# Performance work log

Measured on AMD Instinct MI355X. Metric: run time of the kernel, lower is better.

Reference implementation:

```python
import jax, jax.numpy as jnp
import numpy as np

B, J, HID, INTER, NL = 4096, 16, 128, 64, 4
NEG = -9.0e15
EDGES = [(0,1),(1,2),(2,3),(0,4),(4,5),(5,6),(0,7),(7,8),(8,9),(8,10),(10,11),(11,12),(8,13),(13,14),(14,15)]
GROUPED = [0,7,1,4,2,5,3,6,8,10,9,13,11,14,12,15]  # flattened nodes_group


def _adjacency_nonzeros():
    A = np.zeros((J, J), np.float32)
    for i, j in EDGES:
        A[i, j] = 1.0
        A[j, i] = 1.0
    A += np.eye(J, dtype=np.float32)
    rows, cols = np.nonzero(A)  # row-major, matches torch adj[mask] = e fill order
    return rows.astype(np.int32), cols.astype(np.int32)


def setup_inputs() -> dict:
    key = jax.random.key(0)
    ks = iter(jax.random.split(key, 64))
    rn = lambda shape, s: jax.random.normal(next(ks), shape, jnp.float32) * s
    rows, cols = _adjacency_nonzeros()
    nnz = rows.shape[0]  # 46
    inp = dict(
        x=jax.random.normal(next(ks), (B, J, 2), jnp.float32),
        # input SemGraphConv (2 -> HID) + its BatchNorm
        gc_in_W=rn((2, 2, HID), 0.7), gc_in_e=1.0 + rn((nnz,), 0.3), gc_in_b=rn((HID,), 0.05),
        bn_in_g=1.0 + rn((HID,), 0.05), bn_in_b=rn((HID,), 0.05),
        # 4 residual blocks x 2 graph convs (HID -> HID)
        W_res=rn((2 * NL, 2, HID, HID), 0.08), e_res=1.0 + rn((2 * NL, nnz), 0.3),
        b_res=rn((2 * NL, HID), 0.05),
        bng_res=1.0 + rn((2 * NL, HID), 0.05), bnb_res=rn((2 * NL, HID), 0.05),
        # 5 GraphNonLocal blocks (1 after input + 1 per residual block)
        nl_g_w=rn((NL + 1, INTER, HID), 0.08), nl_g_b=rn((NL + 1, INTER), 0.05),
        nl_t_w=rn((NL + 1, INTER, HID), 0.08), nl_t_b=rn((NL + 1, INTER), 0.05),
        nl_p_w=rn((NL + 1, INTER, HID), 0.08), nl_p_b=rn((NL + 1, INTER), 0.05),
        nl_cp_w=rn((NL + 1, 2 * INTER), 0.08),  # concat_project 1x1 conv, no bias
        nl_W_w=rn((NL + 1, HID, INTER), 0.08), nl_W_b=rn((NL + 1, HID), 0.05),
        nl_bn_g=1.0 + rn((NL + 1, HID), 0.05), nl_bn_b=rn((NL + 1, HID), 0.05),
        # output SemGraphConv (HID -> 3)
        gc_out_W=rn((2, HID, 3), 0.08), gc_out_e=1.0 + rn((nnz,), 0.3), gc_out_b=rn((3,), 0.05),
        # integer constants
        mask_rows=jnp.asarray(rows), mask_cols=jnp.asarray(cols),
        grouped_order=jnp.asarray(GROUPED, jnp.int32),
        restored_order=jnp.asarray(np.argsort(GROUPED), jnp.int32),
    )
    return inp


def reference(x, gc_in_W, gc_in_e, gc_in_b, bn_in_g, bn_in_b,
              W_res, e_res, b_res, bng_res, bnb_res,
              nl_g_w, nl_g_b, nl_t_w, nl_t_b, nl_p_w, nl_p_b,
              nl_cp_w, nl_W_w, nl_W_b, nl_bn_g, nl_bn_b,
              gc_out_W, gc_out_e, gc_out_b,
              mask_rows, mask_cols, grouped_order, restored_order):
    eye = jnp.eye(J, dtype=x.dtype)

    def gconv(h, W, e, b):
        # h: [B, J, F]
        h0 = jnp.einsum('bjf,fo->bjo', h, W[0])
        h1 = jnp.einsum('bjf,fo->bjo', h, W[1])
        logits = jnp.full((J, J), NEG, h.dtype).at[mask_rows, mask_cols].set(e)
        adj = jax.nn.softmax(logits, axis=1)
        diag = jnp.diagonal(adj)                     # adj*I picks diagonal scaling
        off = adj * (1.0 - eye)
        return diag[None, :, None] * h0 + jnp.einsum('ij,bjo->bio', off, h1) + b

    def bn(h, g, bta, axes):
        # training-mode BatchNorm (biased variance), per-channel
        m = h.mean(axes, keepdims=True)
        v = h.var(axes, keepdims=True)
        return (h - m) * jax.lax.rsqrt(v + 1e-5) * g + bta

    def graph_conv(h, W, e, b, gm, gb):
        h = gconv(h, W, e, b)
        h = bn(h, gm[None, None, :], gb[None, None, :], (0, 1))
        return jax.nn.relu(h)

    def nonlocal_block(h, i):
        xo = h[:, grouped_order]          # [B, J, C] regroup joints
        xc = xo.transpose(0, 2, 1)        # [B, C, J]
        conv = lambda w, bb: jnp.einsum('oc,bcj->boj', w, xc) + bb[None, :, None]
        pool = lambda t: t.reshape(B, INTER, J // 2, 2).max(-1)   # MaxPool1d(k=2)
        gx = pool(conv(nl_g_w[i], nl_g_b[i]))                     # [B, I, J/2]
        th = conv(nl_t_w[i], nl_t_b[i])                           # [B, I, J]
        ph = pool(conv(nl_p_w[i], nl_p_b[i]))                     # [B, I, J/2]
        wt, wp = nl_cp_w[i][:INTER], nl_cp_w[i][INTER:]
        # concat_project 1x1 conv over concat(theta,phi) decomposes into a sum
        f = jax.nn.relu(jnp.einsum('bch,c->bh', th, wt)[:, :, None]
                        + jnp.einsum('bcw,c->bw', ph, wp)[:, None, :])  # [B, J, J/2]
        f = f / (J // 2)
        y = jnp.einsum('bhw,bcw->bch', f, gx)                     # [B, I, J]
        Wy = jnp.einsum('oc,bch->boh', nl_W_w[i], y) + nl_W_b[i][None, :, None]
        Wy = bn(Wy, nl_bn_g[i][None, :, None], nl_bn_b[i][None, :, None], (0, 2))
        z = Wy + xc
        return z.transpose(0, 2, 1)[:, restored_order]

    out = graph_conv(x, gc_in_W, gc_in_e, gc_in_b, bn_in_g, bn_in_b)
    out = nonlocal_block(out, 0)
    for i in range(NL):
        res = out
        out = graph_conv(out, W_res[2 * i], e_res[2 * i], b_res[2 * i], bng_res[2 * i], bnb_res[2 * i])
        out = graph_conv(out, W_res[2 * i + 1], e_res[2 * i + 1], b_res[2 * i + 1], bng_res[2 * i + 1], bnb_res[2 * i + 1])
        out = res + out
        out = nonlocal_block(out, i + 1)
    return gconv(out, gc_out_W, gc_out_e, gc_out_b)  # [B, J, 3]
```

## Files before the change

kernel.cpp:

```cpp
#include <hip/hip_runtime.h>

#define B 4096
#define J 16
#define HID 128
#define INTER 64
#define NLAYERS 4
#define NEGV -9000000000000000.0f
#define ELEMS ((size_t)B*16*128)
#define NREP 16
#define SLOT 4096

typedef __attribute__((ext_vector_type(8))) short short8;
typedef __attribute__((ext_vector_type(4))) float f32x4;

static __device__ __forceinline__ unsigned short f2bf(float x) {
    unsigned u = __float_as_uint(x);
    unsigned r = u + 0x7fffu + ((u >> 16) & 1u);
    return (unsigned short)(r >> 16);
}
static __device__ __forceinline__ void splitbf(float x, unsigned short& h, unsigned short& l) {
    h = f2bf(x);
    float hf = __uint_as_float((unsigned)h << 16);
    l = f2bf(x - hf);
}
static __device__ __forceinline__ void splitbf4(float4 v, uint2& hh, uint2& ll) {
    unsigned short h0,l0,h1,l1,h2,l2,h3,l3;
    splitbf(v.x,h0,l0); splitbf(v.y,h1,l1); splitbf(v.z,h2,l2); splitbf(v.w,h3,l3);
    hh = make_uint2((unsigned)h0 | ((unsigned)h1<<16), (unsigned)h2 | ((unsigned)h3<<16));
    ll = make_uint2((unsigned)l0 | ((unsigned)l1<<16), (unsigned)l2 | ((unsigned)l3<<16));
}
static __device__ __forceinline__ f32x4 mfma16(short8 a, short8 b, f32x4 c) {
    return __builtin_amdgcn_mfma_f32_16x16x32_bf16(a, b, c, 0, 0, 0);
}
static __device__ __forceinline__ f32x4 mfma_split(short8 ah, short8 al,
                                                   short8 bh, short8 bl, f32x4 acc) {
    acc = mfma16(ah, bh, acc);
    acc = mfma16(ah, bl, acc);
    acc = mfma16(al, bh, acc);
    return acc;
}
static __device__ __forceinline__ float bfpair(unsigned short h, unsigned short l) {
    return __uint_as_float((unsigned)h << 16) + __uint_as_float((unsigned)l << 16);
}

__global__ void adj_kernel(const float* __restrict__ e_in,
                           const float* __restrict__ e_res,
                           const float* __restrict__ e_out,
                           const int* __restrict__ rows,
                           const int* __restrict__ cols, int nnz,
                           float* __restrict__ off_all,
                           float* __restrict__ diag_all) {
    int m = blockIdx.x;
    int i = threadIdx.x;
    const float* e = (m == 0) ? e_in : (m <= 8) ? e_res + (size_t)(m - 1) * nnz : e_out;
    float l[16];
    for (int j = 0; j < 16; j++) l[j] = NEGV;
    for (int k = 0; k < nnz; k++)
        if (rows[k] == i) l[cols[k]] = e[k];
    float mx = l[0];
    for (int j = 1; j < 16; j++) mx = fmaxf(mx, l[j]);
    float ex[16], s = 0.f;
    for (int j = 0; j < 16; j++) { ex[j] = expf(l[j] - mx); s += ex[j]; }
    float inv = 1.f / s;
    for (int j = 0; j < 16; j++) {
        float a = ex[j] * inv;
        if (j == i) { diag_all[m * 16 + i] = a; a = 0.f; }
        off_all[m * 256 + i * 16 + j] = a;
    }
}

#define WB_N   262144
#define NLW_N  122880
#define NLWW_N 40960
__global__ void prep_w_kernel(const float* __restrict__ W_res,
                              const float* __restrict__ g_w, const float* __restrict__ t_w,
                              const float* __restrict__ p_w, const float* __restrict__ W_w,
                              unsigned short* __restrict__ Wbh, unsigned short* __restrict__ Wbl,
                              unsigned short* __restrict__ nlwh, unsigned short* __restrict__ nlwl,
                              unsigned short* __restrict__ nlWh, unsigned short* __restrict__ nlWl) {
    int i = blockIdx.x * 256 + threadIdx.x;
    unsigned short h, l;
    if (i < WB_N) {
        int lay = i >> 15, rem = i & 32767, n = rem >> 8, k = rem & 255;
        int d = k >> 7, f = k & 127;
        splitbf(W_res[(((lay << 1) | d) * 128 + f) * 128 + n], h, l);
        Wbh[i] = h; Wbl[i] = l;
    } else if (i < WB_N + NLW_N) {
        int j = i - WB_N;
        int lay = j / 24576, r2 = j % 24576;
        int conv = r2 >> 13, oc = r2 & 8191;
        const float* src = conv == 0 ? g_w : conv == 1 ? t_w : p_w;
        splitbf(src[lay * 8192 + oc], h, l);
        nlwh[j] = h; nlwl[j] = l;
    } else if (i < WB_N + NLW_N + NLWW_N) {
        int j = i - WB_N - NLW_N;
        splitbf(W_w[j], h, l);
        nlWh[j] = h; nlWl[j] = l;
    }
}

__global__ void prep_vt_kernel(const float* __restrict__ t_w, const float* __restrict__ t_b,
                               const float* __restrict__ cp_w,
                               float* __restrict__ vt, float* __restrict__ ct) {
    int l = blockIdx.x, c = threadIdx.x;
    float s = 0.f;
    for (int c2 = 0; c2 < 64; c2++)
        s += cp_w[l * 128 + c2] * t_w[(l * 64 + c2) * 128 + c];
    vt[l * 128 + c] = s;
    if (c == 0) {
        float s2 = 0.f;
        for (int c2 = 0; c2 < 64; c2++) s2 += cp_w[l * 128 + c2] * t_b[l * 64 + c2];
        ct[l] = s2;
    }
}

__global__ void finalize_kernel(const float* __restrict__ slot, float* __restrict__ fin) {
    __shared__ float sh[256];
    int t = threadIdx.x;
    float s = 0.f;
    #pragma unroll
    for (int r = 0; r < NREP; r++) s += slot[r * 256 + t];
    sh[t] = s;
    __syncthreads();
    if (t < 128) {
        float m = sh[t] * (1.f / 65536.f);
        float v = sh[128 + t] * (1.f / 65536.f) - m * m;
        fin[t] = m;
        fin[128 + t] = rsqrtf(v + 1e-5f);
    }
}

__global__ __launch_bounds__(256) void gconv_in_kernel(
        const float* __restrict__ x, const float* __restrict__ W,
        const float* __restrict__ bias, const float* __restrict__ off,
        const float* __restrict__ diag, float* __restrict__ out,
        float* __restrict__ stats_out) {
    __shared__ float xs[16][2];
    __shared__ float gs[16][2];
    __shared__ float red[512];
    int b = blockIdx.x, t = threadIdx.x;
    if (t < 32) xs[t >> 1][t & 1] = x[b * 32 + t];
    __syncthreads();
    if (t < 32) {
        int i = t >> 1, f = t & 1;
        float g = 0.f;
        #pragma unroll
        for (int j = 0; j < 16; j++) g += off[i * 16 + j] * xs[j][f];
        gs[i][f] = g;
    }
    __syncthreads();
    int o = t & 127;
    float w00 = W[o], w01 = W[128 + o], w10 = W[256 + o], w11 = W[384 + o], bo = bias[o];
    float s = 0.f, q = 0.f;
    for (int idx = t; idx < 2048; idx += 256) {
        int i = idx >> 7;
        float v = diag[i] * (xs[i][0] * w00 + xs[i][1] * w01)
                + gs[i][0] * w10 + gs[i][1] * w11 + bo;
        out[(size_t)b * 2048 + idx] = v;
        s += v; q += v * v;
    }
    red[t] = s; red[256 + t] = q;
    __syncthreads();
    float* so = stats_out + (b & (NREP - 1)) * 256;
    if (t < 128) {
        atomicAdd(&so[t], red[t] + red[t + 128]);
        atomicAdd(&so[128 + t], red[256 + t] + red[256 + t + 128]);
    }
}

__global__ __launch_bounds__(256) void gconv_mfma_kernel(
        const float* src, const float* wy,
        const float* __restrict__ fin,
        const float* __restrict__ bn_g, const float* __restrict__ bn_b,
        const int* __restrict__ restored, float* zdst,
        const unsigned short* __restrict__ Wbh,
        const unsigned short* __restrict__ Wbl,
        const float* __restrict__ bias,
        const float* __restrict__ off, const float* __restrict__ diag,
        float* dst, float* __restrict__ stats_out) {
    __shared__ float hraw[16][132];
    __shared__ __align__(16) unsigned short ksh[16][264];
    __shared__ __align__(16) unsigned short ksl[16][264];
    __shared__ float offs[256];
    __shared__ float diags[16];
    int t = threadIdx.x;
    offs[t] = off[t];
    if (t < 16) diags[t] = diag[t];
    int c4 = (4 * t) & 127;
    int r0 = t >> 5;
    float4 m4 = make_float4(0,0,0,0), sc4 = make_float4(0,0,0,0), bb4 = make_float4(0,0,0,0);
    if (fin) {
        m4 = *(const float4*)&fin[c4];
        float4 iv = *(const float4*)&fin[128 + c4];
        float4 g4 = *(const float4*)&bn_g[c4];
        bb4 = *(const float4*)&bn_b[c4];
        sc4 = make_float4(iv.x * g4.x, iv.y * g4.y, iv.z * g4.z, iv.w * g4.w);
    }
    int ro0 = 0, ro1 = 0;
    if (wy) { ro0 = restored[r0]; ro1 = restored[r0 + 8]; }
    int b0 = blockIdx.x;
    const float4* src4 = (const float4*)src;
    const float4* wy4  = (const float4*)wy;
    float4 sv0 = src4[(size_t)b0 * 512 + t];
    float4 sv1 = src4[(size_t)b0 * 512 + 256 + t];
    float4 wv0 = make_float4(0,0,0,0), wv1 = make_float4(0,0,0,0);
    if (wy) {
        wv0 = wy4[(size_t)b0 * 512 + ro0 * 32 + (c4 >> 2)];
        wv1 = wy4[(size_t)b0 * 512 + ro1 * 32 + (c4 >> 2)];
    }
    int wv_ = t >> 6, lane = t & 63;
    int mn = lane & 15, kq = (lane >> 4) << 3, qr = (lane >> 4) << 2;

    for (int s = 0; s < 2; s++) {
        int bb_ = blockIdx.x + s * 2048;
        {
            float4 v = sv0;
            if (wy) {
                v.x += (wv0.x - m4.x) * sc4.x + bb4.x;
                v.y += (wv0.y - m4.y) * sc4.y + bb4.y;
                v.z += (wv0.z - m4.z) * sc4.z + bb4.z;
                v.w += (wv0.w - m4.w) * sc4.w + bb4.w;
                ((float4*)zdst)[(size_t)bb_ * 512 + t] = v;
            } else if (fin) {
                v.x = fmaxf((v.x - m4.x) * sc4.x + bb4.x, 0.f);
                v.y = fmaxf((v.y - m4.y) * sc4.y + bb4.y, 0.f);
                v.z = fmaxf((v.z - m4.z) * sc4.z + bb4.z, 0.f);
                v.w = fmaxf((v.w - m4.w) * sc4.w + bb4.w, 0.f);
            }
            *(float4*)&hraw[r0][c4] = v;
            v = sv1;
            if (wy) {
                v.x += (wv1.x - m4.x) * sc4.x + bb4.x;
                v.y += (wv1.y - m4.y) * sc4.y + bb4.y;
                v.z += (wv1.z - m4.z) * sc4.z + bb4.z;
                v.w += (wv1.w - m4.w) * sc4.w + bb4.w;
                ((float4*)zdst)[(size_t)bb_ * 512 + 256 + t] = v;
            } else if (fin) {
                v.x = fmaxf((v.x - m4.x) * sc4.x + bb4.x, 0.f);
                v.y = fmaxf((v.y - m4.y) * sc4.y + bb4.y, 0.f);
                v.z = fmaxf((v.z - m4.z) * sc4.z + bb4.z, 0.f);
                v.w = fmaxf((v.w - m4.w) * sc4.w + bb4.w, 0.f);
            }
            *(float4*)&hraw[r0 + 8][c4] = v;
        }
        if (s == 0) {
            int b1 = blockIdx.x + 2048;
            sv0 = src4[(size_t)b1 * 512 + t];
            sv1 = src4[(size_t)b1 * 512 + 256 + t];
            if (wy) {
                wv0 = wy4[(size_t)b1 * 512 + ro0 * 32 + (c4 >> 2)];
                wv1 = wy4[(size_t)b1 * 512 + ro1 * 32 + (c4 >> 2)];
            }
        }
        __syncthreads();
        for (int u = t; u < 512; u += 256) {
            int i = u >> 5, f4 = (u & 31) << 2;
            float4 hv = *(const float4*)&hraw[i][f4];
            float4 g = make_float4(0.f, 0.f, 0.f, 0.f);
            #pragma unroll
            for (int j = 0; j < 16; j++) {
                float w = offs[i * 16 + j];
                float4 hj = *(const float4*)&hraw[j][f4];
                g.x += w * hj.x; g.y += w * hj.y; g.z += w * hj.z; g.w += w * hj.w;
            }
            float d = diags[i];
            uint2 hh, ll;
            splitbf4(make_float4(d * hv.x, d * hv.y, d * hv.z, d * hv.w), hh, ll);
            *(uint2*)&ksh[i][f4] = hh;
            *(uint2*)&ksl[i][f4] = ll;
            splitbf4(g, hh, ll);
            *(uint2*)&ksh[i][128 + f4] = hh;
            *(uint2*)&ksl[i][128 + f4] = ll;
        }
        __syncthreads();
        int n0 = wv_ << 5;
        f32x4 acc0 = {0.f, 0.f, 0.f, 0.f}, acc1 = {0.f, 0.f, 0.f, 0.f};
        const unsigned short* wh0 = Wbh + (size_t)(n0 + mn) * 256 + kq;
        const unsigned short* wl0 = Wbl + (size_t)(n0 + mn) * 256 + kq;
        #pragma unroll
        for (int k = 0; k < 8; k++) {
            int k0 = k << 5;
            short8 ah = *(const short8*)&ksh[mn][k0 + kq];
            short8 al = *(const short8*)&ksl[mn][k0 + kq];
            acc0 = mfma_split(ah, al, *(const short8*)(wh0 + k0), *(const short8*)(wl0 + k0), acc0);
            acc1 = mfma_split(ah, al, *(const short8*)(wh0 + 4096 + k0), *(const short8*)(wl0 + 4096 + k0), acc1);
        }
        float bias0 = bias[n0 + mn], bias1 = bias[n0 + 16 + mn];
        float s0 = 0.f, q0 = 0.f, s1 = 0.f, q1 = 0.f;
        #pragma unroll
        for (int r = 0; r < 4; r++) {
            int row = qr + r;
            float v0 = acc0[r] + bias0;
            float v1 = acc1[r] + bias1;
            dst[(size_t)bb_ * 2048 + row * 128 + n0 + mn] = v0;
            dst[(size_t)bb_ * 2048 + row * 128 + n0 + 16 + mn] = v1;
            s0 += v0; q0 += v0 * v0; s1 += v1; q1 += v1 * v1;
        }
        s0 += __shfl_xor(s0, 16); s0 += __shfl_xor(s0, 32);
        q0 += __shfl_xor(q0, 16); q0 += __shfl_xor(q0, 32);
        s1 += __shfl_xor(s1, 16); s1 += __shfl_xor(s1, 32);
        q1 += __shfl_xor(q1, 16); q1 += __shfl_xor(q1, 32);
        float* so = stats_out + (bb_ & (NREP - 1)) * 256;
        if (lane < 16) {
            atomicAdd(&so[n0 + mn], s0);
            atomicAdd(&so[128 + n0 + mn], q0);
            atomicAdd(&so[n0 + 16 + mn], s1);
            atomicAdd(&so[128 + n0 + 16 + mn], q1);
        }
        if (s == 0) __syncthreads();
    }
}

#define CG(conv, o, j) cgbuf[((conv) * 64 + (o)) * 17 + (j)]
#define WYL(o, j)      cgbuf[(o) * 17 + (j)]
__global__ __launch_bounds__(256) void nl_a_kernel(
        const float* tsrc, const float* __restrict__ fin,
        const float* __restrict__ bn_g, const float* __restrict__ bn_b,
        const float* res,
        const unsigned short* __restrict__ nlwh,
        const unsigned short* __restrict__ nlwl,
        const float* __restrict__ g_b, const float* __restrict__ p_b,
        const float* __restrict__ cpw,
        const float* __restrict__ vt, const float* __restrict__ ctp,
        const unsigned short* __restrict__ nlWh,
        const unsigned short* __restrict__ nlWl,
        const float* __restrict__ W_b,
        const int* __restrict__ restored,
        float* hdst, float* wydst, float* __restrict__ wst) {
    __shared__ __align__(16) unsigned short xch[16][136];
    __shared__ __align__(16) unsigned short xcl[16][136];
    __shared__ float cgbuf[2176];
    __shared__ float gx[64][9];
    __shared__ float tvp[16][4], pvp[8][8];
    __shared__ float tv[16], pv[8];
    __shared__ float vtl[128];
    __shared__ __align__(16) unsigned short ybh[16][72];
    __shared__ __align__(16) unsigned short ybl[16][72];
    int b = blockIdx.x, t = threadIdx.x;
    {
        if (t < 128) vtl[t] = vt[t];
        int c4 = (4 * t) & 127;
        float4 m4 = *(const float4*)&fin[c4];
        float4 iv = *(const float4*)&fin[128 + c4];
        float4 g4 = *(const float4*)&bn_g[c4];
        float4 bb4 = *(const float4*)&bn_b[c4];
        float4 sc4 = make_float4(iv.x * g4.x, iv.y * g4.y, iv.z * g4.z, iv.w * g4.w);
        int r0 = t >> 5;
        #pragma unroll
        for (int u = 0; u < 2; u++) {
            int fi = t + 256 * u;
            int r = r0 + 8 * u;
            float4 v = ((const float4*)tsrc)[(size_t)b * 512 + fi];
            v.x = fmaxf((v.x - m4.x) * sc4.x + bb4.x, 0.f);
            v.y = fmaxf((v.y - m4.y) * sc4.y + bb4.y, 0.f);
            v.z = fmaxf((v.z - m4.z) * sc4.z + bb4.z, 0.f);
            v.w = fmaxf((v.w - m4.w) * sc4.w + bb4.w, 0.f);
            if (res) {
                float4 rv = ((const float4*)res)[(size_t)b * 512 + fi];
                v.x += rv.x; v.y += rv.y; v.z += rv.z; v.w += rv.w;
            }
            ((float4*)hdst)[(size_t)b * 512 + fi] = v;
            int rg = restored[r];
            uint2 hh, ll;
            splitbf4(v, hh, ll);
            *(uint2*)&xch[rg][c4] = hh;
            *(uint2*)&xcl[rg][c4] = ll;
        }
    }
    __syncthreads();
    int wv = t >> 6, lane = t & 63;
    int mn = lane & 15, kq = (lane >> 4) << 3, qr = (lane >> 4) << 2;
    {
        short8 bh[4], bl[4];
        #pragma unroll
        for (int s = 0; s < 4; s++) {
            bh[s] = *(const short8*)&xch[mn][s * 32 + kq];
            bl[s] = *(const short8*)&xcl[mn][s * 32 + kq];
        }
        #pragma unroll
        for (int jj = 0; jj < 2; jj++) {
            int jb = wv + jj * 4;
            int conv = jb >> 2;
            int mt = jb & 3;
            int wbase = (conv == 0) ? 0 : 128;
            const unsigned short* aph = nlwh + (size_t)(wbase + mt * 16 + mn) * 128 + kq;
            const unsigned short* apl = nlwl + (size_t)(wbase + mt * 16 + mn) * 128 + kq;
            f32x4 acc = {0.f, 0.f, 0.f, 0.f};
            #pragma unroll
            for (int s = 0; s < 4; s++)
                acc = mfma_split(*(const short8*)(aph + s * 32), *(const short8*)(apl + s * 32),
                                 bh[s], bl[s], acc);
            const float* bias = (conv == 0) ? g_b : p_b;
            #pragma unroll
            for (int r = 0; r < 4; r++) {
                int o = mt * 16 + qr + r;
                CG(conv, o, mn) = acc[r] + bias[o];
            }
        }
    }
    __syncthreads();
    if (t < 128) {
        for (int u = t; u < 512; u += 128) {
            int c = u >> 3, w2 = u & 7;
            gx[c][w2] = fmaxf(CG(0, c, 2 * w2), CG(0, c, 2 * w2 + 1));
        }
    } else if (t < 192) {
        int u = t - 128, w2 = u & 7, ch = u >> 3;
        float s = 0.f;
        for (int c = ch * 8; c < ch * 8 + 8; c++)
            s += fmaxf(CG(1, c, 2 * w2), CG(1, c, 2 * w2 + 1)) * cpw[64 + c];
        pvp[w2][ch] = s;
    } else {
        int u = t - 192, j = u & 15, ch = u >> 4;
        float s = 0.f;
        int c0 = ch * 32;
        for (int c = c0; c < c0 + 32; c += 2) {
            unsigned hh = *(const unsigned*)&xch[j][c];
            unsigned ll = *(const unsigned*)&xcl[j][c];
            float v0 = bfpair((unsigned short)hh, (unsigned short)ll);
            float v1 = bfpair((unsigned short)(hh >> 16), (unsigned short)(ll >> 16));
            s += vtl[c] * v0 + vtl[c + 1] * v1;
        }
        tvp[j][ch] = s;
    }
    __syncthreads();
    if (t < 16) {
        tv[t] = tvp[t][0] + tvp[t][1] + tvp[t][2] + tvp[t][3] + ctp[0];
    } else if (t < 24) {
        int w2 = t - 16;
        float s = 0.f;
        #pragma unroll
        for (int ch = 0; ch < 8; ch++) s += pvp[w2][ch];
        pv[w2] = s;
    }
    __syncthreads();
    for (int u = t; u < 1024; u += 256) {
        int j = u >> 6, c = u & 63;
        float s = 0.f;
        #pragma unroll
        for (int w2 = 0; w2 < 8; w2++)
            s += fmaxf(tv[j] + pv[w2], 0.f) * gx[c][w2];
        unsigned short h, l;
        splitbf(s * 0.125f, h, l);
        ybh[j][c] = h; ybl[j][c] = l;
    }
    __syncthreads();
    {
        short8 byh0 = *(const short8*)&ybh[mn][kq];
        short8 byh1 = *(const short8*)&ybh[mn][32 + kq];
        short8 byl0 = *(const short8*)&ybl[mn][kq];
        short8 byl1 = *(const short8*)&ybl[mn][32 + kq];
        #pragma unroll
        for (int mm = 0; mm < 2; mm++) {
            int mt = wv * 2 + mm;
            const unsigned short* aph = nlWh + (size_t)(mt * 16 + mn) * 64 + kq;
            const unsigned short* apl = nlWl + (size_t)(mt * 16 + mn) * 64 + kq;
            f32x4 acc = {0.f, 0.f, 0.f, 0.f};
            acc = mfma_split(*(const short8*)aph, *(const short8*)apl, byh0, byl0, acc);
            acc = mfma_split(*(const short8*)(aph + 32), *(const short8*)(apl + 32), byh1, byl1, acc);
            #pragma unroll
            for (int r = 0; r < 4; r++) {
                int o = mt * 16 + qr + r;
                WYL(o, mn) = acc[r] + W_b[o];
            }
        }
    }
    __syncthreads();
    {
        int c = t & 127;
        float s = 0.f, q = 0.f;
        for (int idx = t; idx < 2048; idx += 256) {
            int j = idx >> 7;
            float v = WYL(c, j);
            wydst[(size_t)b * 2048 + idx] = v;
            s += v; q += v * v;
        }
        float* red = &gx[0][0];
        red[t] = s; red[256 + t] = q;
        __syncthreads();
        float* so = wst + (b & (NREP - 1)) * 256;
        if (t < 128) {
            atomicAdd(&so[t], red[t] + red[t + 128]);
            atomicAdd(&so[128 + t], red[256 + t] + red[256 + t + 128]);
        }
    }
}

__global__ __launch_bounds__(256) void gconv_out_kernel(
        const float* __restrict__ h, const float* __restrict__ wy,
        const float* __restrict__ fin,
        const float* __restrict__ nlg, const float* __restrict__ nlb,
        const int* __restrict__ restored,
        const float* __restrict__ W,
        const float* __restrict__ bias, const float* __restrict__ off,
        const float* __restrict__ diag, float* __restrict__ out) {
    __shared__ float hs[16][132];
    __shared__ float gsv[16][132];
    __shared__ float offs[256];
    __shared__ float p0[48][4], p1[48][4];
    int b = blockIdx.x, t = threadIdx.x;
    offs[t] = off[t];
    {
        int c = t & 127;
        float mean = fin[c];
        float inv = fin[128 + c] * nlg[c];
        float bb = nlb[c];
        for (int idx = t; idx < 2048; idx += 256) {
            int r = idx >> 7;
            float wval = wy[(size_t)b * 2048 + restored[r] * 128 + c];
            hs[r][c] = (wval - mean) * inv + bb + h[(size_t)b * 2048 + idx];
        }
    }
    __syncthreads();
    for (int idx = t; idx < 2048; idx += 256) {
        int i = idx >> 7, f = idx & 127;
        float g = 0.f;
        #pragma unroll
        for (int j = 0; j < 16; j++) g += offs[i * 16 + j] * hs[j][f];
        gsv[i][f] = g;
    }
    __syncthreads();
    if (t < 192) {
        int oid = t >> 2, chunk = t & 3;
        int i = oid / 3, o = oid % 3;
        float a0 = 0.f, a1 = 0.f;
        int f0 = chunk * 32;
        for (int f = f0; f < f0 + 32; f++) {
            a0 += hs[i][f] * W[f * 3 + o];
            a1 += gsv[i][f] * W[384 + f * 3 + o];
        }
        p0[oid][chunk] = a0; p1[oid][chunk] = a1;
    }
    __syncthreads();
    if (t < 48) {
        int i = t / 3, o = t % 3;
        float a0 = p0[t][0] + p0[t][1] + p0[t][2] + p0[t][3];
        float a1 = p1[t][0] + p1[t][1] + p1[t][2] + p1[t][3];
        out[(size_t)b * 48 + t] = diag[i] * a0 + a1 + bias[o];
    }
}

extern "C" void kernel_launch(void* const* d_in, const int* in_sizes, int n_in,
                              void* d_out, int out_size, void* d_ws, size_t ws_size,
                              hipStream_t stream) {
    (void)n_in; (void)out_size; (void)ws_size;
    const float* x        = (const float*)d_in[0];
    const float* gc_in_W  = (const float*)d_in[1];
    const float* gc_in_e  = (const float*)d_in[2];
    const float* gc_in_b  = (const float*)d_in[3];
    const float* bn_in_g  = (const float*)d_in[4];
    const float* bn_in_b  = (const float*)d_in[5];
    const float* W_res    = (const float*)d_in[6];
    const float* e_res    = (const float*)d_in[7];
    const float* b_res    = (const float*)d_in[8];
    const float* bng_res  = (const float*)d_in[9];
    const float* bnb_res  = (const float*)d_in[10];
    const float* nl_g_w   = (const float*)d_in[11];
    const float* nl_g_b   = (const float*)d_in[12];
    const float* nl_t_w   = (const float*)d_in[13];
    const float* nl_t_b   = (const float*)d_in[14];
    const float* nl_p_w   = (const float*)d_in[15];
    const float* nl_p_b   = (const float*)d_in[16];
    const float* nl_cp_w  = (const float*)d_in[17];
    const float* nl_W_w   = (const float*)d_in[18];
    const float* nl_W_b   = (const float*)d_in[19];
    const float* nl_bn_g  = (const float*)d_in[20];
    const float* nl_bn_b  = (const float*)d_in[21];
    const float* gc_out_W = (const float*)d_in[22];
    const float* gc_out_e = (const float*)d_in[23];
    const float* gc_out_b = (const float*)d_in[24];
    const int*   mask_rows = (const int*)d_in[25];
    const int*   mask_cols = (const int*)d_in[26];
    const int*   restored  = (const int*)d_in[28];
    int nnz = in_sizes[2];

    float* ws       = (float*)d_ws;
    float* off_all  = ws;
    float* diag_all = ws + 2560;
    float* stats    = ws + 2720;
    float* fin      = ws + 60064;
    float* vt       = ws + 63664;
    float* ct       = ws + 64304;
    unsigned short* Wbh  = (unsigned short*)(ws + 65536);
    unsigned short* Wbl  = Wbh + WB_N;
    unsigned short* nlwh = Wbl + WB_N;
    unsigned short* nlwl = nlwh + NLW_N;
    unsigned short* nlWh = nlwl + NLW_N;
    unsigned short* nlWl = nlWh + NLWW_N;
    float* Z = ws + 491520;
    float* T = Z + ELEMS;

    hipMemsetAsync(stats, 0, 14 * SLOT * sizeof(float), stream);
    adj_kernel<<<10, 16, 0, stream>>>(gc_in_e, e_res, gc_out_e, mask_rows, mask_cols,
                                      nnz, off_all, diag_all);
    prep_w_kernel<<<(WB_N + NLW_N + NLWW_N + 255) / 256, 256, 0, stream>>>(
        W_res, nl_g_w, nl_t_w, nl_p_w, nl_W_w, Wbh, Wbl, nlwh, nlwl, nlWh, nlWl);
    prep_vt_kernel<<<5, 128, 0, stream>>>(nl_t_w, nl_t_b, nl_cp_w, vt, ct);

    gconv_in_kernel<<<B, 256, 0, stream>>>(x, gc_in_W, gc_in_b, off_all, diag_all,
                                           T, stats);
    finalize_kernel<<<1, 256, 0, stream>>>(stats, fin);
    nl_a_kernel<<<B, 256, 0, stream>>>(T, fin, bn_in_g, bn_in_b, nullptr,
                                       nlwh, nlwl, nl_g_b, nl_p_b, nl_cp_w,
                                       vt, ct, nlWh, nlWl, nl_W_b, restored,
                                       Z, T, stats + SLOT);
    finalize_kernel<<<1, 256, 0, stream>>>(stats + SLOT, fin + 256);

    int sl = 1;
    for (int i = 0; i < NLAYERS; i++) {
        int l0 = 2 * i, l1 = 2 * i + 1, li = i + 1;
        gconv_mfma_kernel<<<2048, 256, 0, stream>>>(
            Z, T, fin + (size_t)sl * 256,
            nl_bn_g + i * 128, nl_bn_b + i * 128, restored, Z,
            Wbh + (size_t)l0 * 32768, Wbl + (size_t)l0 * 32768, b_res + l0 * 128,
            off_all + (1 + l0) * 256, diag_all + (1 + l0) * 16, T,
            stats + (size_t)(sl + 1) * SLOT);
        finalize_kernel<<<1, 256, 0, stream>>>(stats + (size_t)(sl + 1) * SLOT,
                                               fin + (size_t)(sl + 1) * 256);
        gconv_mfma_kernel<<<2048, 256, 0, stream>>>(
            T, nullptr, fin + (size_t)(sl + 1) * 256,
            bng_res + l0 * 128, bnb_res + l0 * 128, nullptr, nullptr,
            Wbh + (size_t)l1 * 32768, Wbl + (size_t)l1 * 32768, b_res + l1 * 128,
            off_all + (1 + l1) * 256, diag_all + (1 + l1) * 16, T,
            stats + (size_t)(sl + 2) * SLOT);
        finalize_kernel<<<1, 256, 0, stream>>>(stats + (size_t)(sl + 2) * SLOT,
                                               fin + (size_t)(sl + 2) * 256);
        nl_a_kernel<<<B, 256, 0, stream>>>(
            T, fin + (size_t)(sl + 2) * 256,
            bng_res + l1 * 128, bnb_res + l1 * 128, Z,
            nlwh + li * 24576, nlwl + li * 24576,
            nl_g_b + li * 64, nl_p_b + li * 64, nl_cp_w + li * 128,
            vt + li * 128, ct + li, nlWh + li * 8192, nlWl + li * 8192,
            nl_W_b + li * 128, restored, Z, T,
            stats + (size_t)(sl + 3) * SLOT);
        finalize_kernel<<<1, 256, 0, stream>>>(stats + (size_t)(sl + 3) * SLOT,
                                               fin + (size_t)(sl + 3) * 256);
        sl += 3;
    }
    gconv_out_kernel<<<B, 256, 0, stream>>>(Z, T, fin + (size_t)sl * 256,
                                            nl_bn_g + NLAYERS * 128, nl_bn_b + NLAYERS * 128,
                                            restored, gc_out_W, gc_out_b,
                                            off_all + 9 * 256, diag_all + 9 * 16,
                                            (float*)d_out);
}
```

Measured before the change: 930.6 us.

## Process multiple batches per block with prefetch in gconv and nonlocal kernels

gconv_mfma_kernel now handles four batch items per block (1024 blocks) and nl_a_kernel handles two (2048 blocks). Each loads the next item's inputs into registers while the current one is computed, so global-load latency overlaps with compute and per-block setup is shared. The number of stats replicas doubles to spread atomic contention, and the workspace offsets are shifted to fit. Both kernels get a minimum-occupancy launch bound, and the trailing barrier in the gconv loop is dropped, which risks a shared-memory race between iterations.

After: 2.483 ms. 167% more time.

```diff
diff --git a/kernel.cpp b/kernel.cpp
--- a/kernel.cpp
+++ b/kernel.cpp
@@ -7,8 +7,8 @@
 #define NLAYERS 4
 #define NEGV -9000000000000000.0f
 #define ELEMS ((size_t)B*16*128)
-#define NREP 16
-#define SLOT 4096
+#define NREP 32
+#define SLOT 8192
 
 typedef __attribute__((ext_vector_type(8))) short short8;
 typedef __attribute__((ext_vector_type(4))) float f32x4;
@@ -168,7 +168,7 @@
     }
 }
 
-__global__ __launch_bounds__(256) void gconv_mfma_kernel(
+__global__ __launch_bounds__(256, 6) void gconv_mfma_kernel(
         const float* src, const float* wy,
         const float* __restrict__ fin,
         const float* __restrict__ bn_g, const float* __restrict__ bn_b,
@@ -198,9 +198,9 @@
     }
     int ro0 = 0, ro1 = 0;
     if (wy) { ro0 = restored[r0]; ro1 = restored[r0 + 8]; }
-    int b0 = blockIdx.x;
     const float4* src4 = (const float4*)src;
     const float4* wy4  = (const float4*)wy;
+    int b0 = blockIdx.x;
     float4 sv0 = src4[(size_t)b0 * 512 + t];
     float4 sv1 = src4[(size_t)b0 * 512 + 256 + t];
     float4 wv0 = make_float4(0,0,0,0), wv1 = make_float4(0,0,0,0);
@@ -211,8 +211,8 @@
     int wv_ = t >> 6, lane = t & 63;
     int mn = lane & 15, kq = (lane >> 4) << 3, qr = (lane >> 4) << 2;
 
-    for (int s = 0; s < 2; s++) {
-        int bb_ = blockIdx.x + s * 2048;
+    for (int s = 0; s < 4; s++) {
+        int bb_ = blockIdx.x + s * 1024;
         {
             float4 v = sv0;
             if (wy) {
@@ -243,8 +243,8 @@
             }
             *(float4*)&hraw[r0 + 8][c4] = v;
         }
-        if (s == 0) {
-            int b1 = blockIdx.x + 2048;
+        if (s < 3) {
+            int b1 = blockIdx.x + (s + 1) * 1024;
             sv0 = src4[(size_t)b1 * 512 + t];
             sv1 = src4[(size_t)b1 * 512 + 256 + t];
             if (wy) {
@@ -307,13 +307,12 @@
             atomicAdd(&so[n0 + 16 + mn], s1);
             atomicAdd(&so[128 + n0 + 16 + mn], q1);
         }
-        if (s == 0) __syncthreads();
     }
 }
 
 #define CG(conv, o, j) cgbuf[((conv) * 64 + (o)) * 17 + (j)]
 #define WYL(o, j)      cgbuf[(o) * 17 + (j)]
-__global__ __launch_bounds__(256) void nl_a_kernel(
+__global__ __launch_bounds__(256, 6) void nl_a_kernel(
         const float* tsrc, const float* __restrict__ fin,
         const float* __restrict__ bn_g, const float* __restrict__ bn_b,
         const float* res,
@@ -336,152 +335,178 @@
     __shared__ float vtl[128];
     __shared__ __align__(16) unsigned short ybh[16][72];
     __shared__ __align__(16) unsigned short ybl[16][72];
-    int b = blockIdx.x, t = threadIdx.x;
-    {
-        if (t < 128) vtl[t] = vt[t];
-        int c4 = (4 * t) & 127;
-        float4 m4 = *(const float4*)&fin[c4];
-        float4 iv = *(const float4*)&fin[128 + c4];
-        float4 g4 = *(const float4*)&bn_g[c4];
-        float4 bb4 = *(const float4*)&bn_b[c4];
-        float4 sc4 = make_float4(iv.x * g4.x, iv.y * g4.y, iv.z * g4.z, iv.w * g4.w);
-        int r0 = t >> 5;
-        #pragma unroll
-        for (int u = 0; u < 2; u++) {
-            int fi = t + 256 * u;
-            int r = r0 + 8 * u;
-            float4 v = ((const float4*)tsrc)[(size_t)b * 512 + fi];
+    int t = threadIdx.x;
+    if (t < 128) vtl[t] = vt[t];
+    int c4 = (4 * t) & 127;
+    int r0 = t >> 5;
+    int rg0 = restored[r0], rg1 = restored[r0 + 8];
+    float ctv = ctp[0];
+    float4 m4 = *(const float4*)&fin[c4];
+    float4 iv = *(const float4*)&fin[128 + c4];
+    float4 g4 = *(const float4*)&bn_g[c4];
+    float4 bb4 = *(const float4*)&bn_b[c4];
+    float4 sc4 = make_float4(iv.x * g4.x, iv.y * g4.y, iv.z * g4.z, iv.w * g4.w);
+    const float4* tsrc4 = (const float4*)tsrc;
+    const float4* res4  = (const float4*)res;
+    int wv = t >> 6, lane = t & 63;
+    int mn = lane & 15, kq = (lane >> 4) << 3, qr = (lane >> 4) << 2;
+    int b0 = blockIdx.x;
+    float4 sv0 = tsrc4[(size_t)b0 * 512 + t];
+    float4 sv1 = tsrc4[(size_t)b0 * 512 + 256 + t];
+    float4 rv0 = make_float4(0,0,0,0), rv1 = make_float4(0,0,0,0);
+    if (res) {
+        rv0 = res4[(size_t)b0 * 512 + t];
+        rv1 = res4[(size_t)b0 * 512 + 256 + t];
+    }
+
+    for (int s = 0; s < 2; s++) {
+        int b = blockIdx.x + s * 2048;
+        {
+            float4 v = sv0;
             v.x = fmaxf((v.x - m4.x) * sc4.x + bb4.x, 0.f);
             v.y = fmaxf((v.y - m4.y) * sc4.y + bb4.y, 0.f);
             v.z = fmaxf((v.z - m4.z) * sc4.z + bb4.z, 0.f);
             v.w = fmaxf((v.w - m4.w) * sc4.w + bb4.w, 0.f);
-            if (res) {
-                float4 rv = ((const float4*)res)[(size_t)b * 512 + fi];
-                v.x += rv.x; v.y += rv.y; v.z += rv.z; v.w += rv.w;
-            }
-            ((float4*)hdst)[(size_t)b * 512 + fi] = v;
-            int rg = restored[r];
+            if (res) { v.x += rv0.x; v.y += rv0.y; v.z += rv0.z; v.w += rv0.w; }
+            ((float4*)hdst)[(size_t)b * 512 + t] = v;
             uint2 hh, ll;
             splitbf4(v, hh, ll);
-            *(uint2*)&xch[rg][c4] = hh;
-            *(uint2*)&xcl[rg][c4] = ll;
-        }
-    }
-    __syncthreads();
-    int wv = t >> 6, lane = t & 63;
-    int mn = lane & 15, kq = (lane >> 4) << 3, qr = (lane >> 4) << 2;
-    {
-        short8 bh[4], bl[4];
-        #pragma unroll
-        for (int s = 0; s < 4; s++) {
-            bh[s] = *(const short8*)&xch[mn][s * 32 + kq];
-            bl[s] = *(const short8*)&xcl[mn][s * 32 + kq];
-        }
-        #pragma unroll
-        for (int jj = 0; jj < 2; jj++) {
-            int jb = wv + jj * 4;
-            int conv = jb >> 2;
-            int mt = jb & 3;
-            int wbase = (conv == 0) ? 0 : 128;
-            const unsigned short* aph = nlwh + (size_t)(wbase + mt * 16 + mn) * 128 + kq;
-            const unsigned short* apl = nlwl + (size_t)(wbase + mt * 16 + mn) * 128 + kq;
-            f32x4 acc = {0.f, 0.f, 0.f, 0.f};
+            *(uint2*)&xch[rg0][c4] = hh;
+            *(uint2*)&xcl[rg0][c4] = ll;
+            v = sv1;
+            v.x = fmaxf((v.x - m4.x) * sc4.x + bb4.x, 0.f);
+            v.y = fmaxf((v.y - m4.y) * sc4.y + bb4.y, 0.f);
+            v.z = fmaxf((v.z - m4.z) * sc4.z + bb4.z, 0.f);
+            v.w = fmaxf((v.w - m4.w) * sc4.w + bb4.w, 0.f);
+            if (res) { v.x += rv1.x; v.y += rv1.y; v.z += rv1.z; v.w += rv1.w; }
+            ((float4*)hdst)[(size_t)b * 512 + 256 + t] = v;
+            splitbf4(v, hh, ll);
+            *(uint2*)&xch[rg1][c4] = hh;
+            *(uint2*)&xcl[rg1][c4] = ll;
+        }
+        if (s == 0) {
+            int b1 = blockIdx.x + 2048;
+            sv0 = tsrc4[(size_t)b1 * 512 + t];
+            sv1 = tsrc4[(size_t)b1 * 512 + 256 + t];
+            if (res) {
+                rv0 = res4[(size_t)b1 * 512 + t];
+                rv1 = res4[(size_t)b1 * 512 + 256 + t];
+            }
+        }
+        __syncthreads();
+        {
+            short8 bh[4], bl[4];
             #pragma unroll
-            for (int s = 0; s < 4; s++)
-                acc = mfma_split(*(const short8*)(aph + s * 32), *(const short8*)(apl + s * 32),
-                                 bh[s], bl[s], acc);
-            const float* bias = (conv == 0) ? g_b : p_b;
+            for (int k = 0; k < 4; k++) {
+                bh[k] = *(const short8*)&xch[mn][k * 32 + kq];
+                bl[k] = *(const short8*)&xcl[mn][k * 32 + kq];
+            }
             #pragma unroll
-            for (int r = 0; r < 4; r++) {
-                int o = mt * 16 + qr + r;
-                CG(conv, o, mn) = acc[r] + bias[o];
-            }
-        }
-    }
-    __syncthreads();
-    if (t < 128) {
-        for (int u = t; u < 512; u += 128) {
-            int c = u >> 3, w2 = u & 7;
-            gx[c][w2] = fmaxf(CG(0, c, 2 * w2), CG(0, c, 2 * w2 + 1));
-        }
-    } else if (t < 192) {
-        int u = t - 128, w2 = u & 7, ch = u >> 3;
-        float s = 0.f;
-        for (int c = ch * 8; c < ch * 8 + 8; c++)
-            s += fmaxf(CG(1, c, 2 * w2), CG(1, c, 2 * w2 + 1)) * cpw[64 + c];
-        pvp[w2][ch] = s;
-    } else {
-        int u = t - 192, j = u & 15, ch = u >> 4;
-        float s = 0.f;
-        int c0 = ch * 32;
-        for (int c = c0; c < c0 + 32; c += 2) {
-            unsigned hh = *(const unsigned*)&xch[j][c];
-            unsigned ll = *(const unsigned*)&xcl[j][c];
-            float v0 = bfpair((unsigned short)hh, (unsigned short)ll);
-            float v1 = bfpair((unsigned short)(hh >> 16), (unsigned short)(ll >> 16));
-            s += vtl[c] * v0 + vtl[c + 1] * v1;
-        }
-        tvp[j][ch] = s;
-    }
-    __syncthreads();
-    if (t < 16) {
-        tv[t] = tvp[t][0] + tvp[t][1] + tvp[t][2] + tvp[t][3] + ctp[0];
-    } else if (t < 24) {
-        int w2 = t - 16;
-        float s = 0.f;
-        #pragma unroll
-        for (int ch = 0; ch < 8; ch++) s += pvp[w2][ch];
-        pv[w2] = s;
-    }
-    __syncthreads();
-    for (int u = t; u < 1024; u += 256) {
-        int j = u >> 6, c = u & 63;
-        float s = 0.f;
-        #pragma unroll
-        for (int w2 = 0; w2 < 8; w2++)
-            s += fmaxf(tv[j] + pv[w2], 0.f) * gx[c][w2];
-        unsigned short h, l;
-        splitbf(s * 0.125f, h, l);
-        ybh[j][c] = h; ybl[j][c] = l;
-    }
-    __syncthreads();
-    {
-        short8 byh0 = *(const short8*)&ybh[mn][kq];
-        short8 byh1 = *(const short8*)&ybh[mn][32 + kq];
-        short8 byl0 = *(const short8*)&ybl[mn][kq];
-        short8 byl1 = *(const short8*)&ybl[mn][32 + kq];
-        #pragma unroll
-        for (int mm = 0; mm < 2; mm++) {
-            int mt = wv * 2 + mm;
-            const unsigned short* aph = nlWh + (size_t)(mt * 16 + mn) * 64 + kq;
-            const unsigned short* apl = nlWl + (size_t)(mt * 16 + mn) * 64 + kq;
-            f32x4 acc = {0.f, 0.f, 0.f, 0.f};
-            acc = mfma_split(*(const short8*)aph, *(const short8*)apl, byh0, byl0, acc);
-            acc = mfma_split(*(const short8*)(aph + 32), *(const short8*)(apl + 32), byh1, byl1, acc);
+            for (int jj = 0; jj < 2; jj++) {
+                int jb = wv + jj * 4;
+                int conv = jb >> 2;
+                int mt = jb & 3;
+                int wbase = (conv == 0) ? 0 : 128;
+                const unsigned short* aph = nlwh + (size_t)(wbase + mt * 16 + mn) * 128 + kq;
+                const unsigned short* apl = nlwl + (size_t)(wbase + mt * 16 + mn) * 128 + kq;
+                f32x4 acc = {0.f, 0.f, 0.f, 0.f};
+                #pragma unroll
+                for (int k = 0; k < 4; k++)
+                    acc = mfma_split(*(const short8*)(aph + k * 32), *(const short8*)(apl + k * 32),
+                                     bh[k], bl[k], acc);
+                const float* bias = (conv == 0) ? g_b : p_b;
+                #pragma unroll
+                for (int r = 0; r < 4; r++) {
+                    int o = mt * 16 + qr + r;
+                    CG(conv, o, mn) = acc[r] + bias[o];
+                }
+            }
+        }
+        __syncthreads();
+        if (t < 128) {
+            for (int u = t; u < 512; u += 128) {
+                int c = u >> 3, w2 = u & 7;
+                gx[c][w2] = fmaxf(CG(0, c, 2 * w2), CG(0, c, 2 * w2 + 1));
+            }
+        } else if (t < 192) {
+            int u = t - 128, w2 = u & 7, ch = u >> 3;
+            float ss = 0.f;
+            for (int c = ch * 8; c < ch * 8 + 8; c++)
+                ss += fmaxf(CG(1, c, 2 * w2), CG(1, c, 2 * w2 + 1)) * cpw[64 + c];
+            pvp[w2][ch] = ss;
+        } else {
+            int u = t - 192, j = u & 15, ch = u >> 4;
+            float ss = 0.f;
+            int c0 = ch * 32;
+            for (int c = c0; c < c0 + 32; c += 2) {
+                unsigned hh = *(const unsigned*)&xch[j][c];
+                unsigned ll = *(const unsigned*)&xcl[j][c];
+                float v0 = bfpair((unsigned short)hh, (unsigned short)ll);
+                float v1 = bfpair((unsigned short)(hh >> 16), (unsigned short)(ll >> 16));
+                ss += vtl[c] * v0 + vtl[c + 1] * v1;
+            }
+            tvp[j][ch] = ss;
+        }
+        __syncthreads();
+        if (t < 16) {
+            tv[t] = tvp[t][0] + tvp[t][1] + tvp[t][2] + tvp[t][3] + ctv;
+        } else if (t < 24) {
+            int w2 = t - 16;
+            float ss = 0.f;
             #pragma unroll
-            for (int r = 0; r < 4; r++) {
-                int o = mt * 16 + qr + r;
-                WYL(o, mn) = acc[r] + W_b[o];
-            }
-        }
-    }
-    __syncthreads();
-    {
-        int c = t & 127;
-        float s = 0.f, q = 0.f;
-        for (int idx = t; idx < 2048; idx += 256) {
-            int j = idx >> 7;
-            float v = WYL(c, j);
-            wydst[(size_t)b * 2048 + idx] = v;
-            s += v; q += v * v;
-        }
-        float* red = &gx[0][0];
-        red[t] = s; red[256 + t] = q;
-        __syncthreads();
-        float* so = wst + (b & (NREP - 1)) * 256;
-        if (t < 128) {
-            atomicAdd(&so[t], red[t] + red[t + 128]);
-            atomicAdd(&so[128 + t], red[256 + t] + red[256 + t + 128]);
+            for (int ch = 0; ch < 8; ch++) ss += pvp[w2][ch];
+            pv[w2] = ss;
+        }
+        __syncthreads();
+        for (int u = t; u < 1024; u += 256) {
+            int j = u >> 6, c = u & 63;
+            float ss = 0.f;
+            #pragma unroll
+            for (int w2 = 0; w2 < 8; w2++)
+                ss += fmaxf(tv[j] + pv[w2], 0.f) * gx[c][w2];
+            unsigned short h, l;
+            splitbf(ss * 0.125f, h, l);
+            ybh[j][c] = h; ybl[j][c] = l;
+        }
+        __syncthreads();
+        {
+            short8 byh0 = *(const short8*)&ybh[mn][kq];
+            short8 byh1 = *(const short8*)&ybh[mn][32 + kq];
+            short8 byl0 = *(const short8*)&ybl[mn][kq];
+            short8 byl1 = *(const short8*)&ybl[mn][32 + kq];
+            #pragma unroll
+            for (int mm = 0; mm < 2; mm++) {
+                int mt = wv * 2 + mm;
+                const unsigned short* aph = nlWh + (size_t)(mt * 16 + mn) * 64 + kq;
+                const unsigned short* apl = nlWl + (size_t)(mt * 16 + mn) * 64 + kq;
+                f32x4 acc = {0.f, 0.f, 0.f, 0.f};
+                acc = mfma_split(*(const short8*)aph, *(const short8*)apl, byh0, byl0, acc);
+                acc = mfma_split(*(const short8*)(aph + 32), *(const short8*)(apl + 32), byh1, byl1, acc);
+                #pragma unroll
+                for (int r = 0; r < 4; r++) {
+                    int o = mt * 16 + qr + r;
+                    WYL(o, mn) = acc[r] + W_b[o];
+                }
+            }
+        }
+        __syncthreads();
+        {
+            int c = t & 127;
+            float ss = 0.f, qq = 0.f;
+            for (int idx = t; idx < 2048; idx += 256) {
+                int j = idx >> 7;
+                float v = WYL(c, j);
+                wydst[(size_t)b * 2048 + idx] = v;
+                ss += v; qq += v * v;
+            }
+            float* red = &gx[0][0];
+            red[t] = ss; red[256 + t] = qq;
+            __syncthreads();
+            float* so = wst + (b & (NREP - 1)) * 256;
+            if (t < 128) {
+                atomicAdd(&so[t], red[t] + red[t + 128]);
+                atomicAdd(&so[128 + t], red[256 + t] + red[256 + t + 128]);
+            }
         }
     }
 }
@@ -578,16 +603,16 @@
     float* off_all  = ws;
     float* diag_all = ws + 2560;
     float* stats    = ws + 2720;
-    float* fin      = ws + 60064;
-    float* vt       = ws + 63664;
-    float* ct       = ws + 64304;
-    unsigned short* Wbh  = (unsigned short*)(ws + 65536);
+    float* fin      = ws + 117408;
+    float* vt       = ws + 120992;
+    float* ct       = ws + 121632;
+    unsigned short* Wbh  = (unsigned short*)(ws + 122880);
     unsigned short* Wbl  = Wbh + WB_N;
     unsigned short* nlwh = Wbl + WB_N;
     unsigned short* nlwl = nlwh + NLW_N;
     unsigned short* nlWh = nlwl + NLW_N;
     unsigned short* nlWl = nlWh + NLWW_N;
-    float* Z = ws + 491520;
+    float* Z = ws + 548864;
     float* T = Z + ELEMS;
 
     hipMemsetAsync(stats, 0, 14 * SLOT * sizeof(float), stream);
@@ -600,16 +625,16 @@
     gconv_in_kernel<<<B, 256, 0, stream>>>(x, gc_in_W, gc_in_b, off_all, diag_all,
                                            T, stats);
     finalize_kernel<<<1, 256, 0, stream>>>(stats, fin);
-    nl_a_kernel<<<B, 256, 0, stream>>>(T, fin, bn_in_g, bn_in_b, nullptr,
-                                       nlwh, nlwl, nl_g_b, nl_p_b, nl_cp_w,
-                                       vt, ct, nlWh, nlWl, nl_W_b, restored,
-                                       Z, T, stats + SLOT);
+    nl_a_kernel<<<2048, 256, 0, stream>>>(T, fin, bn_in_g, bn_in_b, nullptr,
+                                          nlwh, nlwl, nl_g_b, nl_p_b, nl_cp_w,
+                                          vt, ct, nlWh, nlWl, nl_W_b, restored,
+                                          Z, T, stats + SLOT);
     finalize_kernel<<<1, 256, 0, stream>>>(stats + SLOT, fin + 256);
 
     int sl = 1;
     for (int i = 0; i < NLAYERS; i++) {
         int l0 = 2 * i, l1 = 2 * i + 1, li = i + 1;
-        gconv_mfma_kernel<<<2048, 256, 0, stream>>>(
+        gconv_mfma_kernel<<<1024, 256, 0, stream>>>(
             Z, T, fin + (size_t)sl * 256,
             nl_bn_g + i * 128, nl_bn_b + i * 128, restored, Z,
             Wbh + (size_t)l0 * 32768, Wbl + (size_t)l0 * 32768, b_res + l0 * 128,
@@ -617,7 +642,7 @@
             stats + (size_t)(sl + 1) * SLOT);
         finalize_kernel<<<1, 256, 0, stream>>>(stats + (size_t)(sl + 1) * SLOT,
                                                fin + (size_t)(sl + 1) * 256);
-        gconv_mfma_kernel<<<2048, 256, 0, stream>>>(
+        gconv_mfma_kernel<<<1024, 256, 0, stream>>>(
             T, nullptr, fin + (size_t)(sl + 1) * 256,
             bng_res + l0 * 128, bnb_res + l0 * 128, nullptr, nullptr,
             Wbh + (size_t)l1 * 32768, Wbl + (size_t)l1 * 32768, b_res + l1 * 128,
@@ -625,7 +650,7 @@
             stats + (size_t)(sl + 2) * SLOT);
         finalize_kernel<<<1, 256, 0, stream>>>(stats + (size_t)(sl + 2) * SLOT,
                                                fin + (size_t)(sl + 2) * 256);
-        nl_a_kernel<<<B, 256, 0, stream>>>(
+        nl_a_kernel<<<2048, 256, 0, stream>>>(
             T, fin + (size_t)(sl + 2) * 256,
             bng_res + l1 * 128, bnb_res + l1 * 128, Z,
             nlwh + li * 24576, nlwl + li * 24576,
```
